# Kernel tuning notes

Hardware: AMD Instinct MI355X
Metric: run time of the kernel (lower is better)

## Reference

```python
import jax, jax.numpy as jnp
import numpy as np

B, NIN, DIN, M, DOUT = 256, 64, 128, 32, 128
SCALE = 1.0 / np.sqrt(DOUT)  # 1/sqrt(out_d_capsules)


def setup_inputs() -> dict:
    key = jax.random.key(0)
    k1, k2, k3 = jax.random.split(key, 3)
    w_const = float(np.sqrt(M / (DIN * NIN)))  # weight_init_const
    return {
        "x": jax.random.normal(k1, (B, NIN, DIN), dtype=jnp.float32),
        "current_act": jax.random.uniform(k2, (B, NIN), dtype=jnp.float32),
        "W": w_const * jax.random.normal(k3, (NIN, DIN, M, DOUT), dtype=jnp.float32),
        "num_iter": 3,
    }


def reference(x, current_act, W, num_iter):
    # Initial pass: next_capsule_value is None -> q0 = softmax(zeros) = 1/M uniform
    # einsum('nm,bna,namd->bmd', q0, x, W) with uniform q0 == mean over m-weighting = /M
    ncv = jnp.einsum('bna,namd->bmd', x, W) / M  # [B, M, Dout]
    q = jnp.full((B, NIN, M), 1.0 / M, dtype=x.dtype)  # query_key from init step
    # Routing iterations (act_type='EM' -> next_act is None; dp=0 -> no dropout)
    for _ in range(max(1, num_iter)):
        logits = jnp.einsum('bna,namd,bmd->bnm', x, W, ncv) * SCALE  # [B, Nin, M]
        q = jax.nn.softmax(logits, axis=2)
        ncv = jnp.einsum('bnm,bna,namd,bn->bmd', q, x, W, current_act)
    # Per-pair votes and routed class embeddings
    votes = jnp.einsum('bna,namd->bnmd', x, W)          # [B, Nin, M, Dout]
    weights = q * current_act[:, :, None]               # [B, Nin, M]
    route_class_emb = weights[..., None] * votes        # [B, Nin, M, Dout]
    return ncv, q, route_class_emb
```

## Files before the change

kernel.cpp:

```cpp
#include <hip/hip_runtime.h>
#include <math.h>

#define B_    256
#define NIN_  64
#define DIN_  128
#define M_    32
#define DOUT_ 128
#define NUM_ITER 3

static constexpr float SCALE = 0.0883883476483184405501f;

typedef __attribute__((ext_vector_type(8))) short bf16x8;
typedef __attribute__((ext_vector_type(4))) float f32x4;

__device__ __forceinline__ unsigned short f2bf(float f) {
    union { float f; unsigned u; } c; c.f = f;
    unsigned r = c.u + 0x7FFFu + ((c.u >> 16) & 1u);
    return (unsigned short)(r >> 16);
}
__device__ __forceinline__ float lo2f(unsigned u) {
    union { unsigned u; float f; } c; c.u = u << 16; return c.f;
}
__device__ __forceinline__ float hi2f(unsigned u) {
    union { unsigned u; float f; } c; c.u = u & 0xffff0000u; return c.f;
}


__global__ __launch_bounds__(256) void k_votes_mfma(const float* __restrict__ x,
                                                    const float* __restrict__ W,
                                                    float* __restrict__ route) {
    const int n    = blockIdx.x;
    const int j0   = blockIdx.y * 512;
    const int t    = threadIdx.x;
    const int w    = t >> 6;
    const int lane = t & 63;
    const int l15  = lane & 15;
    const int l4   = lane >> 4;

    __shared__ __align__(16) char lds[49152];
    char* xbuf = lds;
    char* wbuf = lds + 32768;

    bf16x8 af[4][4];

    for (int h = 0; h < 2; ++h) {
        {
            const int col4 = (t & 15) * 4;
            const int roff = t >> 4;
            const int boff = col4 * 2;
            for (int p = 0; p < 16; ++p) {
                int row = p * 16 + roff;
                const float* src = x + (size_t)row * (NIN_ * DIN_) + (size_t)n * DIN_ + h * 64 + col4;
                float4 v = *(const float4*)src;
                uint2 pk;
                pk.x = (unsigned)f2bf(v.x) | ((unsigned)f2bf(v.y) << 16);
                pk.y = (unsigned)f2bf(v.z) | ((unsigned)f2bf(v.w) << 16);
                *(uint2*)(xbuf + row * 128 + (boff ^ ((row & 7) << 4))) = pk;
            }
        }
        __syncthreads();
#pragma unroll
        for (int mf = 0; mf < 4; ++mf) {
            int row = w * 64 + mf * 16 + l15;
            int sw  = (row & 7) << 4;
#pragma unroll
            for (int kfh = 0; kfh < 2; ++kfh) {
                int kbyte = kfh * 64 + l4 * 16;
                af[mf][h * 2 + kfh] = *(const bf16x8*)(xbuf + row * 128 + (kbyte ^ sw));
            }
        }
        __syncthreads();
    }

    const int jlane = t & 63;
    const int kg    = t >> 6;

    for (int jt = 0; jt < 8; ++jt) {
        {
            const int jcol = j0 + jt * 64 + jlane;
            const float* Wp = W + (size_t)n * (DIN_ * M_ * DOUT_) + jcol;
            const int sw = (jlane & 7) << 4;
#pragma unroll
            for (int c = 0; c < 4; ++c) {
                int kbase = kg * 32 + c * 8;
                unsigned pk[4];
#pragma unroll
                for (int r = 0; r < 4; ++r) {
                    float f0 = __builtin_nontemporal_load(&Wp[(size_t)(kbase + 2 * r)     * 4096]);
                    float f1 = __builtin_nontemporal_load(&Wp[(size_t)(kbase + 2 * r + 1) * 4096]);
                    pk[r] = (unsigned)f2bf(f0) | ((unsigned)f2bf(f1) << 16);
                }
                *(uint4*)(wbuf + jlane * 256 + ((kbase * 2) ^ sw)) = *(uint4*)pk;
            }
        }
        __syncthreads();

        f32x4 acc[4][4];
#pragma unroll
        for (int mf = 0; mf < 4; ++mf)
#pragma unroll
            for (int nf = 0; nf < 4; ++nf) acc[mf][nf] = (f32x4){0.f, 0.f, 0.f, 0.f};

#pragma unroll
        for (int kf = 0; kf < 4; ++kf) {
            bf16x8 bfr[4];
            int kbyte = kf * 64 + l4 * 16;
#pragma unroll
            for (int nf = 0; nf < 4; ++nf) {
                int col = nf * 16 + l15;
                bfr[nf] = *(const bf16x8*)(wbuf + col * 256 + (kbyte ^ ((col & 7) << 4)));
            }
#pragma unroll
            for (int mf = 0; mf < 4; ++mf)
#pragma unroll
                for (int nf = 0; nf < 4; ++nf)
                    acc[mf][nf] = __builtin_amdgcn_mfma_f32_16x16x32_bf16(af[mf][kf], bfr[nf], acc[mf][nf], 0, 0, 0);
        }
        __syncthreads();

#pragma unroll
        for (int mf = 0; mf < 4; ++mf) {
#pragma unroll
            for (int nf = 0; nf < 4; ++nf) {
                const int jb = nf * 16 + l15;
#pragma unroll
                for (int r = 0; r < 4; ++r) {
                    const int b = w * 64 + mf * 16 + l4 * 4 + r;
                    *(unsigned short*)(xbuf + b * 128 + ((jb * 2) ^ ((b & 12) << 3))) = f2bf(acc[mf][nf][r]);
                }
            }
        }
        __syncthreads();

        {
            char* vout = (char*)route;
            const size_t obase = (size_t)n * 16384 + (size_t)(j0 + jt * 64) * 2;
#pragma unroll
            for (int p = 0; p < 8; ++p) {
                const int b = p * 32 + (t >> 3);
                const int c = (t & 7) * 16;
                uint4 val = *(const uint4*)(xbuf + b * 128 + (c ^ ((b & 12) << 3)));
                *(uint4*)(vout + (size_t)b * 1048576 + obase + c) = val;
            }
        }
        __syncthreads();
    }
}

__global__ __launch_bounds__(256) void k_ncv0(const float* __restrict__ route,
                                              float* __restrict__ ncv) {
    const int tid = blockIdx.x * 256 + threadIdx.x;
    const int b   = tid >> 9;
    const int jq  = (tid & 511) * 8;
    const char* vp = (const char*)route + (size_t)b * 1048576 + (size_t)jq * 2;
    float s[8] = {0.f, 0.f, 0.f, 0.f, 0.f, 0.f, 0.f, 0.f};
    for (int n = 0; n < 64; ++n) {
        uint4 v = *(const uint4*)(vp + (size_t)n * 16384);
        s[0] += lo2f(v.x); s[1] += hi2f(v.x);
        s[2] += lo2f(v.y); s[3] += hi2f(v.y);
        s[4] += lo2f(v.z); s[5] += hi2f(v.z);
        s[6] += lo2f(v.w); s[7] += hi2f(v.w);
    }
    float* op = ncv + (size_t)b * 4096 + jq;
    f32x4 o0 = {s[0] * (1.0f/32.0f), s[1] * (1.0f/32.0f), s[2] * (1.0f/32.0f), s[3] * (1.0f/32.0f)};
    f32x4 o1 = {s[4] * (1.0f/32.0f), s[5] * (1.0f/32.0f), s[6] * (1.0f/32.0f), s[7] * (1.0f/32.0f)};
    *(f32x4*)op       = o0;
    *(f32x4*)(op + 4) = o1;
}

__global__ __launch_bounds__(512, 2) void k_iter(
        float* __restrict__ route, const float* __restrict__ act,
        const float* __restrict__ in0, const float* __restrict__ in1,
        long i_bs, long i_hs, float iscale,
        float* __restrict__ pout, long p_hoff, long p_bs, long p_hs,
        float* __restrict__ q_out, int wrf, int nh) {
    const int b    = blockIdx.x;
    const int h    = blockIdx.y;
    const int t    = threadIdx.x;
    const int base = t * 8;
    const int m    = t >> 4;
    const int n0   = h * nh;
    const int nch  = nh >> 2;

    __shared__ float logits_s[4][32];
    __shared__ float w_s[4][32];
    __shared__ float sact[NIN_];
    if (t < 64) sact[t] = act[b * 64 + t];

    const char* vb = (const char*)route + (size_t)b * 1048576;
    const long jh  = (long)(t >> 8);
    const long jl  = (long)(base & 2047);

    float ncvp[8], acc[8];
    {
        const float* a = in0 + (long)b * i_bs + jh * i_hs + jl;
        const float* c = in1 + (long)b * i_bs + jh * i_hs + jl;
#pragma unroll
        for (int i = 0; i < 8; ++i) ncvp[i] = (a[i] + c[i]) * iscale;
    }
#pragma unroll
    for (int i = 0; i < 8; ++i) acc[i] = 0.f;

    uint4 vA[4], vB[4];

#define LOADC(DST, CC) { \
    _Pragma("unroll") \
    for (int r = 0; r < 4; ++r) \
        DST[r] = *(const uint4*)(vb + (size_t)(n0 + (CC) * 4 + r) * 16384 + (size_t)t * 16); }

#define PH_A(V) { \
    _Pragma("unroll") \
    for (int r = 0; r < 4; ++r) { \
        float p = 0.f; \
        p = fmaf(lo2f(V[r].x), ncvp[0], p); p = fmaf(hi2f(V[r].x), ncvp[1], p); \
        p = fmaf(lo2f(V[r].y), ncvp[2], p); p = fmaf(hi2f(V[r].y), ncvp[3], p); \
        p = fmaf(lo2f(V[r].z), ncvp[4], p); p = fmaf(hi2f(V[r].z), ncvp[5], p); \
        p = fmaf(lo2f(V[r].w), ncvp[6], p); p = fmaf(hi2f(V[r].w), ncvp[7], p); \
        p += __shfl_xor(p, 1); p += __shfl_xor(p, 2); \
        p += __shfl_xor(p, 4); p += __shfl_xor(p, 8); \
        if ((t & 15) == 0) logits_s[r][m] = p * SCALE; \
    } }

#define PH_B(CC) { \
    if (t < 128) { \
        const int rr = t >> 5; const int ln = t & 31; \
        float l  = logits_s[rr][ln]; \
        float mx = l; \
        mx = fmaxf(mx, __shfl_xor(mx, 1));  mx = fmaxf(mx, __shfl_xor(mx, 2)); \
        mx = fmaxf(mx, __shfl_xor(mx, 4));  mx = fmaxf(mx, __shfl_xor(mx, 8)); \
        mx = fmaxf(mx, __shfl_xor(mx, 16)); \
        float e  = __expf(l - mx); \
        float su = e; \
        su += __shfl_xor(su, 1);  su += __shfl_xor(su, 2); \
        su += __shfl_xor(su, 4);  su += __shfl_xor(su, 8);  su += __shfl_xor(su, 16); \
        float qv = e / su; \
        const int ng = n0 + (CC) * 4 + rr; \
        w_s[rr][ln] = qv * sact[ng]; \
        if (wrf) q_out[(size_t)b * 2048 + (size_t)ng * 32 + ln] = qv; \
    } }

#define PH_C(V, CC) { \
    _Pragma("unroll") \
    for (int r = 0; r < 4; ++r) { \
        const float wg = w_s[r][m]; \
        float f0 = lo2f(V[r].x), f1 = hi2f(V[r].x), f2 = lo2f(V[r].y), f3 = hi2f(V[r].y); \
        acc[0] = fmaf(wg, f0, acc[0]); acc[1] = fmaf(wg, f1, acc[1]); \
        acc[2] = fmaf(wg, f2, acc[2]); acc[3] = fmaf(wg, f3, acc[3]); \
        float f4 = lo2f(V[r].z), f5 = hi2f(V[r].z), f6 = lo2f(V[r].w), f7 = hi2f(V[r].w); \
        acc[4] = fmaf(wg, f4, acc[4]); acc[5] = fmaf(wg, f5, acc[5]); \
        acc[6] = fmaf(wg, f6, acc[6]); acc[7] = fmaf(wg, f7, acc[7]); \
        if (wrf) { \
            f32x4 r0 = {wg * f0, wg * f1, wg * f2, wg * f3}; \
            f32x4 r1 = {wg * f4, wg * f5, wg * f6, wg * f7}; \
            float* rp = route + (size_t)b * 262144 + (size_t)(n0 + (CC) * 4 + r) * 4096 + base; \
            *(f32x4*)rp       = r0; \
            *(f32x4*)(rp + 4) = r1; \
        } \
    } }

#define PROC(V, CC) { PH_A(V); __syncthreads(); PH_B(CC); __syncthreads(); PH_C(V, CC); }

    LOADC(vA, 0);
    LOADC(vB, 1);
    for (int cc = 0; cc < nch; cc += 2) {
        PROC(vA, cc);
        if (cc + 2 < nch) { LOADC(vA, cc + 2); }
        PROC(vB, cc + 1);
        if (cc + 3 < nch) { LOADC(vB, cc + 3); }
    }

    float* pp = pout + (long)h * p_hoff + (long)b * p_bs + jh * p_hs + jl;
    f32x4 o0 = {acc[0], acc[1], acc[2], acc[3]};
    f32x4 o1 = {acc[4], acc[5], acc[6], acc[7]};
    *(f32x4*)pp       = o0;
    *(f32x4*)(pp + 4) = o1;

#undef LOADC
#undef PH_A
#undef PH_B
#undef PH_C
#undef PROC
}

__global__ __launch_bounds__(256) void k_fold(const float* __restrict__ s0,
                                              const float* __restrict__ s1,
                                              float* __restrict__ dst,
                                              long bs, long hs) {
    const int tid = blockIdx.x * 256 + threadIdx.x;
    const int b   = tid >> 10;
    const int jq  = (tid & 1023) << 2;
    const long off = (long)b * bs + (long)(jq >> 11) * hs + (jq & 2047);
    f32x4 x = *(const f32x4*)(s0 + off);
    f32x4 y = *(const f32x4*)(s1 + off);
    f32x4 o = {x.x + y.x, x.y + y.y, x.z + y.z, x.w + y.w};
    *(f32x4*)(dst + (size_t)b * 4096 + jq) = o;
}

extern "C" void kernel_launch(void* const* d_in, const int* in_sizes, int n_in,
                              void* d_out, int out_size, void* d_ws, size_t ws_size,
                              hipStream_t stream) {
    const float* x   = (const float*)d_in[0];
    const float* act = (const float*)d_in[1];
    const float* W   = (const float*)d_in[2];
    (void)in_sizes; (void)n_in; (void)out_size;

    float* out   = (float*)d_out;
    float* ncv   = out;
    float* q     = out + 1048576;
    float* route = out + 1572864;

    float* spot0 = route + 0 * 2048 + 512;
    spot0 = route + 0 * 8192 + 2048;
    float* spot1 = route + 1 * 8192 + 2048;
    float* spot2 = route + 2 * 8192 + 2048;
    float* spot3 = route + 3 * 8192 + 2048;

    const bool split3 = (d_ws != nullptr) && (ws_size >= (size_t)2 * 1048576 * 4);
    float* wsp = (float*)d_ws;

    hipLaunchKernelGGL(k_votes_mfma, dim3(64, 8), dim3(256), 0, stream, x, W, route);
    hipLaunchKernelGGL(k_ncv0, dim3(512), dim3(256), 0, stream, route, ncv);

    hipLaunchKernelGGL(k_iter, dim3(256, 2), dim3(512), 0, stream,
                       route, act, ncv, ncv, (long)4096, (long)2048, 0.5f,
                       spot0, (long)8192, (long)262144, (long)4096, q, 0, 32);
    hipLaunchKernelGGL(k_iter, dim3(256, 2), dim3(512), 0, stream,
                       route, act, spot0, spot1, (long)262144, (long)4096, 1.0f,
                       spot2, (long)8192, (long)262144, (long)4096, q, 0, 32);
    hipLaunchKernelGGL(k_fold, dim3(1024), dim3(256), 0, stream,
                       spot2, spot3, ncv, (long)262144, (long)4096);

    if (split3) {
        hipLaunchKernelGGL(k_iter, dim3(256, 2), dim3(512), 0, stream,
                           route, act, ncv, ncv, (long)4096, (long)2048, 0.5f,
                           wsp, (long)1048576, (long)4096, (long)2048, q, 1, 32);
        hipLaunchKernelGGL(k_fold, dim3(1024), dim3(256), 0, stream,
                           wsp, wsp + 1048576, ncv, (long)4096, (long)2048);
    } else {
        hipLaunchKernelGGL(k_iter, dim3(256, 1), dim3(512), 0, stream,
                           route, act, ncv, ncv, (long)4096, (long)2048, 0.5f,
                           ncv, (long)0, (long)4096, (long)2048, q, 1, 64);
    }
}
```

Before: 249.1 us.

## Split first two routing iterations four ways over Nin; drop workspace split for final pass

Adds k_iter2, which handles 16 input capsules per block with all votes held in registers, and launches it with a 4-way split over Nin. This doubles the block count of the first two routing iterations. Partial sums are stashed in unused route slots and summed by a new 4-input fold kernel. The final iteration now always uses the single-block 64-capsule path instead of the workspace-based 2-way split, which trades parallelism in the last pass for one fewer launch. Holding 16 uint4 values per thread raises register pressure.

```diff
diff --git a/kernel.cpp b/kernel.cpp
--- a/kernel.cpp
+++ b/kernel.cpp
@@ -168,6 +168,116 @@
     *(f32x4*)(op + 4) = o1;
 }
 
+__global__ __launch_bounds__(512, 2) void k_iter2(
+        float* __restrict__ route, const float* __restrict__ act,
+        const float* __restrict__ i0, const float* __restrict__ i1,
+        const float* __restrict__ i2, const float* __restrict__ i3,
+        long i_bs, long i_hs, float iscale,
+        float* __restrict__ pout, long p_hoff, long p_bs, long p_hs,
+        float* __restrict__ q_out, int wrf) {
+    const int b    = blockIdx.x;
+    const int h    = blockIdx.y;
+    const int t    = threadIdx.x;
+    const int base = t * 8;
+    const int mj   = t >> 4;
+    const int n0   = h * 16;
+
+    __shared__ float logits_s[16][32];
+    __shared__ float w_s[16][32];
+    __shared__ float sact[NIN_];
+    if (t < 64) sact[t] = act[b * 64 + t];
+
+    const char* vb = (const char*)route + (size_t)b * 1048576;
+
+    uint4 v[16];
+#pragma unroll
+    for (int r = 0; r < 16; ++r)
+        v[r] = *(const uint4*)(vb + (size_t)(n0 + r) * 16384 + (size_t)t * 16);
+
+    const long jh = (long)(t >> 8);
+    const long jl = (long)(base & 2047);
+    float ncvp[8];
+    {
+        const long off = (long)b * i_bs + jh * i_hs + jl;
+#pragma unroll
+        for (int i = 0; i < 8; ++i)
+            ncvp[i] = (i0[off + i] + i1[off + i] + i2[off + i] + i3[off + i]) * iscale;
+    }
+
+#pragma unroll
+    for (int r = 0; r < 16; ++r) {
+        float p = 0.f;
+        p = fmaf(lo2f(v[r].x), ncvp[0], p); p = fmaf(hi2f(v[r].x), ncvp[1], p);
+        p = fmaf(lo2f(v[r].y), ncvp[2], p); p = fmaf(hi2f(v[r].y), ncvp[3], p);
+        p = fmaf(lo2f(v[r].z), ncvp[4], p); p = fmaf(hi2f(v[r].z), ncvp[5], p);
+        p = fmaf(lo2f(v[r].w), ncvp[6], p); p = fmaf(hi2f(v[r].w), ncvp[7], p);
+        p += __shfl_xor(p, 1); p += __shfl_xor(p, 2);
+        p += __shfl_xor(p, 4); p += __shfl_xor(p, 8);
+        if ((t & 15) == 0) logits_s[r][mj] = p * SCALE;
+    }
+    __syncthreads();
+
+    {
+        const int nl  = t >> 5;
+        const int msm = t & 31;
+        const int ng  = n0 + nl;
+        float l  = logits_s[nl][msm];
+        float mx = l;
+        mx = fmaxf(mx, __shfl_xor(mx, 1));  mx = fmaxf(mx, __shfl_xor(mx, 2));
+        mx = fmaxf(mx, __shfl_xor(mx, 4));  mx = fmaxf(mx, __shfl_xor(mx, 8));
+        mx = fmaxf(mx, __shfl_xor(mx, 16));
+        float e  = __expf(l - mx);
+        float su = e;
+        su += __shfl_xor(su, 1);  su += __shfl_xor(su, 2);
+        su += __shfl_xor(su, 4);  su += __shfl_xor(su, 8);  su += __shfl_xor(su, 16);
+        float qv = e / su;
+        w_s[nl][msm] = qv * sact[ng];
+        if (wrf) q_out[(size_t)b * 2048 + (size_t)ng * 32 + msm] = qv;
+    }
+    __syncthreads();
+
+    float acc[8] = {0.f, 0.f, 0.f, 0.f, 0.f, 0.f, 0.f, 0.f};
+#pragma unroll
+    for (int r = 0; r < 16; ++r) {
+        const float wg = w_s[r][mj];
+        float f0 = lo2f(v[r].x), f1 = hi2f(v[r].x), f2 = lo2f(v[r].y), f3 = hi2f(v[r].y);
+        float f4 = lo2f(v[r].z), f5 = hi2f(v[r].z), f6 = lo2f(v[r].w), f7 = hi2f(v[r].w);
+        acc[0] = fmaf(wg, f0, acc[0]); acc[1] = fmaf(wg, f1, acc[1]);
+        acc[2] = fmaf(wg, f2, acc[2]); acc[3] = fmaf(wg, f3, acc[3]);
+        acc[4] = fmaf(wg, f4, acc[4]); acc[5] = fmaf(wg, f5, acc[5]);
+        acc[6] = fmaf(wg, f6, acc[6]); acc[7] = fmaf(wg, f7, acc[7]);
+        if (wrf) {
+            f32x4 r0 = {wg * f0, wg * f1, wg * f2, wg * f3};
+            f32x4 r1 = {wg * f4, wg * f5, wg * f6, wg * f7};
+            float* rp = route + (size_t)b * 262144 + (size_t)(n0 + r) * 4096 + base;
+            *(f32x4*)rp       = r0;
+            *(f32x4*)(rp + 4) = r1;
+        }
+    }
+
+    float* pp = pout + (long)h * p_hoff + (long)b * p_bs + jh * p_hs + jl;
+    f32x4 o0 = {acc[0], acc[1], acc[2], acc[3]};
+    f32x4 o1 = {acc[4], acc[5], acc[6], acc[7]};
+    *(f32x4*)pp       = o0;
+    *(f32x4*)(pp + 4) = o1;
+}
+
+__global__ __launch_bounds__(256) void k_fold4(const float* __restrict__ src,
+                                               float* __restrict__ dst,
+                                               long bs, long hs, long ss) {
+    const int tid = blockIdx.x * 256 + threadIdx.x;
+    const int b   = tid >> 10;
+    const int jq  = (tid & 1023) << 2;
+    const long off = (long)b * bs + (long)(jq >> 11) * hs + (jq & 2047);
+    f32x4 s0 = *(const f32x4*)(src + off);
+    f32x4 s1 = *(const f32x4*)(src + off + ss);
+    f32x4 s2 = *(const f32x4*)(src + off + 2 * ss);
+    f32x4 s3 = *(const f32x4*)(src + off + 3 * ss);
+    f32x4 o = {s0.x + s1.x + s2.x + s3.x, s0.y + s1.y + s2.y + s3.y,
+               s0.z + s1.z + s2.z + s3.z, s0.w + s1.w + s2.w + s3.w};
+    *(f32x4*)(dst + (size_t)b * 4096 + jq) = o;
+}
+
 __global__ __launch_bounds__(512, 2) void k_iter(
         float* __restrict__ route, const float* __restrict__ act,
         const float* __restrict__ in0, const float* __restrict__ in1,
@@ -223,8 +333,8 @@
 
 #define PH_B(CC) { \
     if (t < 128) { \
-        const int rr = t >> 5; const int ln = t & 31; \
-        float l  = logits_s[rr][ln]; \
+        const int rr = t >> 5; const int ln2 = t & 31; \
+        float l  = logits_s[rr][ln2]; \
         float mx = l; \
         mx = fmaxf(mx, __shfl_xor(mx, 1));  mx = fmaxf(mx, __shfl_xor(mx, 2)); \
         mx = fmaxf(mx, __shfl_xor(mx, 4));  mx = fmaxf(mx, __shfl_xor(mx, 8)); \
@@ -235,8 +345,8 @@
         su += __shfl_xor(su, 4);  su += __shfl_xor(su, 8);  su += __shfl_xor(su, 16); \
         float qv = e / su; \
         const int ng = n0 + (CC) * 4 + rr; \
-        w_s[rr][ln] = qv * sact[ng]; \
-        if (wrf) q_out[(size_t)b * 2048 + (size_t)ng * 32 + ln] = qv; \
+        w_s[rr][ln2] = qv * sact[ng]; \
+        if (wrf) q_out[(size_t)b * 2048 + (size_t)ng * 32 + ln2] = qv; \
     } }
 
 #define PH_C(V, CC) { \
@@ -282,63 +392,35 @@
 #undef PROC
 }
 
-__global__ __launch_bounds__(256) void k_fold(const float* __restrict__ s0,
-                                              const float* __restrict__ s1,
-                                              float* __restrict__ dst,
-                                              long bs, long hs) {
-    const int tid = blockIdx.x * 256 + threadIdx.x;
-    const int b   = tid >> 10;
-    const int jq  = (tid & 1023) << 2;
-    const long off = (long)b * bs + (long)(jq >> 11) * hs + (jq & 2047);
-    f32x4 x = *(const f32x4*)(s0 + off);
-    f32x4 y = *(const f32x4*)(s1 + off);
-    f32x4 o = {x.x + y.x, x.y + y.y, x.z + y.z, x.w + y.w};
-    *(f32x4*)(dst + (size_t)b * 4096 + jq) = o;
-}
-
 extern "C" void kernel_launch(void* const* d_in, const int* in_sizes, int n_in,
                               void* d_out, int out_size, void* d_ws, size_t ws_size,
                               hipStream_t stream) {
     const float* x   = (const float*)d_in[0];
     const float* act = (const float*)d_in[1];
     const float* W   = (const float*)d_in[2];
-    (void)in_sizes; (void)n_in; (void)out_size;
+    (void)in_sizes; (void)n_in; (void)d_ws; (void)ws_size; (void)out_size;
 
     float* out   = (float*)d_out;
     float* ncv   = out;
     float* q     = out + 1048576;
     float* route = out + 1572864;
 
-    float* spot0 = route + 0 * 2048 + 512;
-    spot0 = route + 0 * 8192 + 2048;
-    float* spot1 = route + 1 * 8192 + 2048;
-    float* spot2 = route + 2 * 8192 + 2048;
-    float* spot3 = route + 3 * 8192 + 2048;
-
-    const bool split3 = (d_ws != nullptr) && (ws_size >= (size_t)2 * 1048576 * 4);
-    float* wsp = (float*)d_ws;
+    float* s0 = route + 2048;
+    float* s4 = route + 4 * 8192 + 2048;
 
     hipLaunchKernelGGL(k_votes_mfma, dim3(64, 8), dim3(256), 0, stream, x, W, route);
     hipLaunchKernelGGL(k_ncv0, dim3(512), dim3(256), 0, stream, route, ncv);
 
-    hipLaunchKernelGGL(k_iter, dim3(256, 2), dim3(512), 0, stream,
+    hipLaunchKernelGGL(k_iter2, dim3(256, 4), dim3(512), 0, stream,
+                       route, act, ncv, ncv, ncv, ncv, (long)4096, (long)2048, 0.25f,
+                       s0, (long)8192, (long)262144, (long)4096, q, 0);
+    hipLaunchKernelGGL(k_iter2, dim3(256, 4), dim3(512), 0, stream,
+                       route, act, s0, s0 + 8192, s0 + 16384, s0 + 24576,
+                       (long)262144, (long)4096, 1.0f,
+                       s4, (long)8192, (long)262144, (long)4096, q, 0);
+    hipLaunchKernelGGL(k_fold4, dim3(1024), dim3(256), 0, stream,
+                       s4, ncv, (long)262144, (long)4096, (long)8192);
+    hipLaunchKernelGGL(k_iter, dim3(256, 1), dim3(512), 0, stream,
                        route, act, ncv, ncv, (long)4096, (long)2048, 0.5f,
-                       spot0, (long)8192, (long)262144, (long)4096, q, 0, 32);
-    hipLaunchKernelGGL(k_iter, dim3(256, 2), dim3(512), 0, stream,
-                       route, act, spot0, spot1, (long)262144, (long)4096, 1.0f,
-                       spot2, (long)8192, (long)262144, (long)4096, q, 0, 32);
-    hipLaunchKernelGGL(k_fold, dim3(1024), dim3(256), 0, stream,
-                       spot2, spot3, ncv, (long)262144, (long)4096);
-
-    if (split3) {
-        hipLaunchKernelGGL(k_iter, dim3(256, 2), dim3(512), 0, stream,
-                           route, act, ncv, ncv, (long)4096, (long)2048, 0.5f,
-                           wsp, (long)1048576, (long)4096, (long)2048, q, 1, 32);
-        hipLaunchKernelGGL(k_fold, dim3(1024), dim3(256), 0, stream,
-                           wsp, wsp + 1048576, ncv, (long)4096, (long)2048);
-    } else {
-        hipLaunchKernelGGL(k_iter, dim3(256, 1), dim3(512), 0, stream,
-                           route, act, ncv, ncv, (long)4096, (long)2048, 0.5f,
-                           ncv, (long)0, (long)4096, (long)2048, q, 1, 64);
-    }
-}
+                       ncv, (long)0, (long)4096, (long)2048, q, 1, 64);
+}
```

New measurement: 258.4 us. 3.8% more time.
